# Kernel tuning notes

Hardware: AMD Instinct MI355X
Metric: run time of the kernel (lower is better)

The kernel has to match this reference:

```python
import jax, jax.numpy as jnp
import numpy as np

MARGIN = 1.0
N, D = 4096, 512
NUM_CLASSES = 64


def setup_inputs() -> dict:
    key = jax.random.key(0)
    k1, k2 = jax.random.split(key)
    inputs = jax.random.normal(k1, (N, D), dtype=jnp.float32)
    targets = jax.random.randint(k2, (N,), 0, NUM_CLASSES, dtype=jnp.int64)
    return {"inputs": inputs, "targets": targets}


def reference(inputs, targets):
    n = inputs.shape[0]
    sq = jnp.sum(inputs * inputs, axis=1)  # [n]
    # squared Euclidean distances, clamped at 0 (matches relu in original)
    d2 = jnp.maximum(sq[:, None] + sq[None, :] - 2.0 * (inputs @ inputs.T), 0.0)
    # safe sqrt (zero entries get 0, matching forward; avoids NaN grads)
    dist = jnp.where(d2 > 0, jnp.sqrt(jnp.where(d2 > 0, d2, 1.0)), 0.0)  # [n,n]

    same = targets[:, None] == targets[None, :]
    eye = jnp.eye(n, dtype=bool)
    pos_mask = same & ~eye          # positives, diagonal excluded
    neg_mask = ~same                # negatives (diagonal is same-label, excluded)

    # per-row sum_k exp(margin - d_ik) over negatives  (replaces per-pair loop)
    neg_sum = jnp.sum(jnp.where(neg_mask, jnp.exp(MARGIN - dist), 0.0), axis=1)  # [n]

    # J_ij = log(neg_sum_i + neg_sum_j) + d_ij for positive pairs
    J = jnp.log(neg_sum[:, None] + neg_sum[None, :]) + dist
    triu_pos = jnp.triu(pos_mask)   # loop iterated over upper-triangular positives
    hinge2 = jnp.where(triu_pos, jax.nn.relu(J) ** 2, 0.0)

    # original divides by count of ALL positive entries (both triangles)
    len_p = jnp.sum(pos_mask).astype(jnp.float32)
    return jnp.sum(hinge2) / len_p
```

## Files before the change

kernel.cpp:

```cpp
#include <hip/hip_runtime.h>
#include <math.h>

#define NN 4096
#define DD 512
#define MARGINF 1.0f
#define NCLS 64
#define MAXM 160
#define TRI (MAXM * (MAXM - 1) / 2)
#define NBLK 2080

typedef __attribute__((ext_vector_type(8))) short bf16x8;
typedef __attribute__((ext_vector_type(4))) float f32x4;

#define WS_SQ   0
#define WS_NS   4096
#define WS_LOSS 8192
#define WS_CTR  8193
#define WS_LENP 8194
#define WS_RK   8320
#define WS_MEM  12416
#define WS_XF   32768
#define WS_PD   1081344

__device__ __forceinline__ unsigned short f2bf(float f) {
    unsigned u = __float_as_uint(f);
    u += 0x7fffu + ((u >> 16) & 1u);
    return (unsigned short)(u >> 16);
}

__global__ __launch_bounds__(256) void prep_kernel(const float* __restrict__ X,
                                                   const int* __restrict__ tgt,
                                                   float* __restrict__ ws) {
    __shared__ int tg[NN];
    const int tid = threadIdx.x;
    for (int j = tid; j < NN; j += 256) tg[j] = tgt[j];

    const int wv = tid >> 6, lane = tid & 63;
    const int row = blockIdx.x * 4 + wv;
    const float4* xr = (const float4*)(X + (size_t)row * DD);
    float4 a = xr[2 * lane], b = xr[2 * lane + 1];
    float s = a.x * a.x + a.y * a.y + a.z * a.z + a.w * a.w
            + b.x * b.x + b.y * b.y + b.z * b.z + b.w * b.w;
#pragma unroll
    for (int off = 32; off; off >>= 1) s += __shfl_down(s, off, 64);

    ushort4 pa = {f2bf(a.x), f2bf(a.y), f2bf(a.z), f2bf(a.w)};
    ushort4 pb = {f2bf(b.x), f2bf(b.y), f2bf(b.z), f2bf(b.w)};
    const int r16 = row >> 4, m = row & 15;
    const int kb = lane >> 2, q = lane & 3;
    ushort4* dst = (ushort4*)((unsigned short*)(ws + WS_XF)
                              + ((size_t)(r16 * 16 + kb) * 64 + q * 16 + m) * 8);
    dst[0] = pa;
    dst[1] = pb;

    __syncthreads();
    const int myc = tg[row];
    int cnt = 0;
    for (int j = lane; j < row; j += 64) cnt += (tg[j] == myc) ? 1 : 0;
#pragma unroll
    for (int off = 32; off; off >>= 1) cnt += __shfl_down(cnt, off, 64);
    if (lane == 0) {
        ws[WS_SQ + row] = s;
        ws[WS_NS + row] = 0.0f;
        ((int*)(ws + WS_RK))[row] = cnt;
        if (cnt < MAXM) ((int*)(ws + WS_MEM))[myc * MAXM + cnt] = row;
    }
    if (blockIdx.x == 0 && tid == 0) {
        ws[WS_LOSS] = 0.0f;
        ((unsigned*)ws)[WS_CTR] = 0u;
        ws[WS_LENP] = 0.0f;
    }
}

__global__ __launch_bounds__(256, 5) void negsum_kernel(const int* __restrict__ tgt,
                                                        float* __restrict__ ws) {
    const int bidx = blockIdx.x;
    int bj = (int)((sqrtf(8.0f * (float)bidx + 1.0f) - 1.0f) * 0.5f);
    while (bj * (bj + 1) / 2 > bidx) --bj;
    while ((bj + 1) * (bj + 2) / 2 <= bidx) ++bj;
    const int bi = bidx - bj * (bj + 1) / 2;
    const int i0 = bi * 64, j0 = bj * 64;

    const int tid = threadIdx.x;
    const int w = tid >> 6, lane = tid & 63;
    const int m_ = lane & 15, q = lane >> 4;
    const int wr = (w & 1) * 32, wc = (w >> 1) * 32;
    const unsigned short* Xf = (const unsigned short*)(ws + WS_XF);

    const int air = (i0 + wr) >> 4;
    const int bjr = (j0 + wc) >> 4;
    const unsigned short* pA = Xf + (size_t)air * 8192 + lane * 8;
    const unsigned short* pB = Xf + (size_t)bjr * 8192 + lane * 8;

    f32x4 acc[2][2] = {};
    bf16x8 rgA[3][2], rgB[3][2];
#pragma unroll
    for (int s = 0; s < 2; ++s)
#pragma unroll
        for (int u = 0; u < 2; ++u) {
            rgA[s][u] = *(const bf16x8*)(pA + u * 8192 + s * 512);
            rgB[s][u] = *(const bf16x8*)(pB + u * 8192 + s * 512);
        }
#pragma unroll
    for (int it = 0; it < 16; ++it) {
        const int cur = it % 3, nx = (it + 2) % 3;
        if (it < 14) {
#pragma unroll
            for (int u = 0; u < 2; ++u) {
                rgA[nx][u] = *(const bf16x8*)(pA + u * 8192 + (it + 2) * 512);
                rgB[nx][u] = *(const bf16x8*)(pB + u * 8192 + (it + 2) * 512);
            }
        }
        acc[0][0] = __builtin_amdgcn_mfma_f32_16x16x32_bf16(rgA[cur][0], rgB[cur][0], acc[0][0], 0, 0, 0);
        acc[0][1] = __builtin_amdgcn_mfma_f32_16x16x32_bf16(rgA[cur][0], rgB[cur][1], acc[0][1], 0, 0, 0);
        acc[1][0] = __builtin_amdgcn_mfma_f32_16x16x32_bf16(rgA[cur][1], rgB[cur][0], acc[1][0], 0, 0, 0);
        acc[1][1] = __builtin_amdgcn_mfma_f32_16x16x32_bf16(rgA[cur][1], rgB[cur][1], acc[1][1], 0, 0, 0);
    }

    const float* sq = ws + WS_SQ;
    float* ns = ws + WS_NS;
    const int* rk = (const int*)(ws + WS_RK);
    float* posd = ws + WS_PD;
    float sjv[2]; int tjv[2], jv[2];
#pragma unroll
    for (int v = 0; v < 2; ++v) {
        int j = j0 + wc + v * 16 + m_;
        jv[v] = j;
        sjv[v] = sq[j];
        tjv[v] = tgt[j];
    }
    float colp[2] = {0.0f, 0.0f};
#pragma unroll
    for (int u = 0; u < 2; ++u) {
#pragma unroll
        for (int r = 0; r < 4; ++r) {
            const int i = i0 + wr + u * 16 + q * 4 + r;
            const float si = sq[i];
            const int ti = tgt[i];
            float rp = 0.0f;
#pragma unroll
            for (int v = 0; v < 2; ++v) {
                float d2 = si + sjv[v] - 2.0f * acc[u][v][r];
                float dist = d2 > 0.0f ? sqrtf(d2) : 0.0f;
                if (tjv[v] != ti) {
                    float e = __expf(MARGINF - dist);
                    rp += e;
                    colp[v] += e;
                } else if (i < jv[v]) {
                    int ra = rk[i], rb = rk[jv[v]];
                    if (ra < MAXM && rb < MAXM) {
                        int hi = ra > rb ? ra : rb;
                        int lo = ra > rb ? rb : ra;
                        posd[ti * TRI + hi * (hi - 1) / 2 + lo] = dist;
                    }
                }
            }
            rp += __shfl_xor(rp, 1, 64);
            rp += __shfl_xor(rp, 2, 64);
            rp += __shfl_xor(rp, 4, 64);
            rp += __shfl_xor(rp, 8, 64);
            if (m_ == 0) atomicAdd(&ns[i], rp);
        }
    }
    if (bi != bj) {
#pragma unroll
        for (int v = 0; v < 2; ++v) {
            float cp = colp[v];
            cp += __shfl_xor(cp, 16, 64);
            cp += __shfl_xor(cp, 32, 64);
            if (q == 0) atomicAdd(&ns[jv[v]], cp);
        }
    }
}

__global__ __launch_bounds__(256) void pair2_kernel(const int* __restrict__ tgt,
                                                    float* __restrict__ ws,
                                                    float* __restrict__ out) {
    __shared__ float wsum[4];
    __shared__ int csum[4];
    __shared__ bool last;
    const int c = blockIdx.x;
    const int tid = threadIdx.x;
    const int wv = tid >> 6, lane = tid & 63;

    int ccount = 0;
    for (int j = tid; j < NN; j += 256) ccount += (tgt[j] == c) ? 1 : 0;
#pragma unroll
    for (int off = 32; off; off >>= 1) ccount += __shfl_down(ccount, off, 64);
    if (lane == 0) csum[wv] = ccount;
    __syncthreads();
    int mc = csum[0] + csum[1] + csum[2] + csum[3];
    if (mc > MAXM) mc = MAXM;
    const int P = mc * (mc - 1) / 2;

    const int* mem = (const int*)(ws + WS_MEM) + c * MAXM;
    const float* pd = ws + WS_PD + c * TRI;
    const float* ns = ws + WS_NS;
    float lsum = 0.0f;
    for (int p = tid; p < P; p += 256) {
        int b = (int)((1.0f + sqrtf(1.0f + 8.0f * (float)p)) * 0.5f);
        while (b * (b - 1) / 2 > p) --b;
        while ((b + 1) * b / 2 <= p) ++b;
        const int a = p - b * (b - 1) / 2;
        const float dist = pd[b * (b - 1) / 2 + a];
        const int i = mem[a], j = mem[b];
        float J = __logf(ns[i] + ns[j]) + dist;
        float h = fmaxf(J, 0.0f);
        lsum += h * h;
    }
#pragma unroll
    for (int off = 32; off; off >>= 1) lsum += __shfl_xor(lsum, off, 64);
    if (lane == 0) wsum[wv] = lsum;
    __syncthreads();
    if (tid == 0) {
        float s = wsum[0] + wsum[1] + wsum[2] + wsum[3];
        if (s != 0.0f) atomicAdd(&ws[WS_LOSS], s);
        atomicAdd(&ws[WS_LENP], (float)(mc * (mc - 1)));
        __threadfence();
        unsigned d = atomicAdd((unsigned*)ws + WS_CTR, 1u);
        last = (d == NCLS - 1);
    }
    __syncthreads();
    if (last && tid == 0) {
        float total = atomicAdd(&ws[WS_LOSS], 0.0f);
        float lp = atomicAdd(&ws[WS_LENP], 0.0f);
        out[0] = total / lp;
    }
}

extern "C" void kernel_launch(void* const* d_in, const int* in_sizes, int n_in,
                              void* d_out, int out_size, void* d_ws, size_t ws_size,
                              hipStream_t stream) {
    const float* X  = (const float*)d_in[0];
    const int*  tgt = (const int*)d_in[1];
    float* ws  = (float*)d_ws;
    float* out = (float*)d_out;

    hipLaunchKernelGGL(prep_kernel, dim3(NN / 4), dim3(256), 0, stream, X, tgt, ws);
    hipLaunchKernelGGL(negsum_kernel, dim3(NBLK), dim3(256), 0, stream, tgt, ws);
    hipLaunchKernelGGL(pair2_kernel, dim3(NCLS), dim3(256), 0, stream, tgt, ws, out);
}
```

Measured before the change: 116.0 us.

## Stage 128x128 Gram tiles through LDS and split pair loss across class slices

The distance/negsum kernel moves from 64x64 tiles loaded directly into registers to 128x128 tiles. Operands are staged into double-buffered LDS with global_load_lds, and each wave computes a 4x4 grid of MFMA tiles, which cuts redundant global reads of the bf16 panels. The pair-loss kernel is also split into 4 slices per class, so 256 blocks replace 64 for more parallelism. In exchange, the larger tiles leave fewer blocks (528) and lower occupancy, and the extra block syncs and register pressure could offset the bandwidth savings.

```diff
diff --git a/kernel.cpp b/kernel.cpp
--- a/kernel.cpp
+++ b/kernel.cpp
@@ -7,7 +7,9 @@
 #define NCLS 64
 #define MAXM 160
 #define TRI (MAXM * (MAXM - 1) / 2)
-#define NBLK 2080
+#define PBLK 32
+#define NBLK2 (PBLK * (PBLK + 1) / 2)
+#define NSLICE 4
 
 typedef __attribute__((ext_vector_type(8))) short bf16x8;
 typedef __attribute__((ext_vector_type(4))) float f32x4;
@@ -72,66 +74,85 @@
     }
 }
 
-__global__ __launch_bounds__(256, 5) void negsum_kernel(const int* __restrict__ tgt,
+__device__ __forceinline__ void stage8(const unsigned short* __restrict__ gpanel,
+                                       int t, int fbase, int lane,
+                                       unsigned short* lbase) {
+#pragma unroll
+    for (int s = 0; s < 8; ++s) {
+        const int fi = fbase + s;
+        const unsigned short* gp =
+            gpanel + ((size_t)((fi >> 1) * 16 + t * 2 + (fi & 1))) * 512 + lane * 8;
+        __builtin_amdgcn_global_load_lds(
+            (const __attribute__((address_space(1))) int*)gp,
+            (__attribute__((address_space(3))) int*)(lbase + fi * 512),
+            16, 0, 0);
+    }
+}
+
+__global__ __launch_bounds__(256, 2) void negsum_kernel(const int* __restrict__ tgt,
                                                         float* __restrict__ ws) {
+    __shared__ unsigned short lds[2][2][16][512];
     const int bidx = blockIdx.x;
     int bj = (int)((sqrtf(8.0f * (float)bidx + 1.0f) - 1.0f) * 0.5f);
     while (bj * (bj + 1) / 2 > bidx) --bj;
     while ((bj + 1) * (bj + 2) / 2 <= bidx) ++bj;
     const int bi = bidx - bj * (bj + 1) / 2;
-    const int i0 = bi * 64, j0 = bj * 64;
+    const int i0 = bi * 128, j0 = bj * 128;
 
     const int tid = threadIdx.x;
     const int w = tid >> 6, lane = tid & 63;
     const int m_ = lane & 15, q = lane >> 4;
-    const int wr = (w & 1) * 32, wc = (w >> 1) * 32;
+    const int wr = (w & 1) * 64, wc = (w >> 1) * 64;
     const unsigned short* Xf = (const unsigned short*)(ws + WS_XF);
 
-    const int air = (i0 + wr) >> 4;
-    const int bjr = (j0 + wc) >> 4;
-    const unsigned short* pA = Xf + (size_t)air * 8192 + lane * 8;
-    const unsigned short* pB = Xf + (size_t)bjr * 8192 + lane * 8;
-
-    f32x4 acc[2][2] = {};
-    bf16x8 rgA[3][2], rgB[3][2];
-#pragma unroll
-    for (int s = 0; s < 2; ++s)
-#pragma unroll
-        for (int u = 0; u < 2; ++u) {
-            rgA[s][u] = *(const bf16x8*)(pA + u * 8192 + s * 512);
-            rgB[s][u] = *(const bf16x8*)(pB + u * 8192 + s * 512);
+    const int ab = w >> 1;
+    const int fbase = (w & 1) * 8;
+    const unsigned short* gpanel = Xf + (size_t)(ab ? bj : bi) * 8 * 8192;
+    unsigned short* lb0 = &lds[0][ab][0][0];
+    unsigned short* lb1 = &lds[1][ab][0][0];
+
+    f32x4 acc[4][4] = {};
+
+    stage8(gpanel, 0, fbase, lane, lb0);
+    __syncthreads();
+#pragma unroll 2
+    for (int t = 0; t < 8; ++t) {
+        const int cur = t & 1;
+        if (t < 7) stage8(gpanel, t + 1, fbase, lane, cur ? lb0 : lb1);
+#pragma unroll
+        for (int kbl = 0; kbl < 2; ++kbl) {
+            bf16x8 af[4], bf[4];
+#pragma unroll
+            for (int u = 0; u < 4; ++u)
+                af[u] = *(const bf16x8*)&lds[cur][0][((w & 1) * 4 + u) * 2 + kbl][lane * 8];
+#pragma unroll
+            for (int v = 0; v < 4; ++v)
+                bf[v] = *(const bf16x8*)&lds[cur][1][((w >> 1) * 4 + v) * 2 + kbl][lane * 8];
+#pragma unroll
+            for (int u = 0; u < 4; ++u)
+#pragma unroll
+                for (int v = 0; v < 4; ++v)
+                    acc[u][v] = __builtin_amdgcn_mfma_f32_16x16x32_bf16(
+                        af[u], bf[v], acc[u][v], 0, 0, 0);
         }
-#pragma unroll
-    for (int it = 0; it < 16; ++it) {
-        const int cur = it % 3, nx = (it + 2) % 3;
-        if (it < 14) {
-#pragma unroll
-            for (int u = 0; u < 2; ++u) {
-                rgA[nx][u] = *(const bf16x8*)(pA + u * 8192 + (it + 2) * 512);
-                rgB[nx][u] = *(const bf16x8*)(pB + u * 8192 + (it + 2) * 512);
-            }
-        }
-        acc[0][0] = __builtin_amdgcn_mfma_f32_16x16x32_bf16(rgA[cur][0], rgB[cur][0], acc[0][0], 0, 0, 0);
-        acc[0][1] = __builtin_amdgcn_mfma_f32_16x16x32_bf16(rgA[cur][0], rgB[cur][1], acc[0][1], 0, 0, 0);
-        acc[1][0] = __builtin_amdgcn_mfma_f32_16x16x32_bf16(rgA[cur][1], rgB[cur][0], acc[1][0], 0, 0, 0);
-        acc[1][1] = __builtin_amdgcn_mfma_f32_16x16x32_bf16(rgA[cur][1], rgB[cur][1], acc[1][1], 0, 0, 0);
+        __syncthreads();
     }
 
     const float* sq = ws + WS_SQ;
     float* ns = ws + WS_NS;
     const int* rk = (const int*)(ws + WS_RK);
     float* posd = ws + WS_PD;
-    float sjv[2]; int tjv[2], jv[2];
-#pragma unroll
-    for (int v = 0; v < 2; ++v) {
+    float sjv[4]; int tjv[4], jv[4];
+#pragma unroll
+    for (int v = 0; v < 4; ++v) {
         int j = j0 + wc + v * 16 + m_;
         jv[v] = j;
         sjv[v] = sq[j];
         tjv[v] = tgt[j];
     }
-    float colp[2] = {0.0f, 0.0f};
-#pragma unroll
-    for (int u = 0; u < 2; ++u) {
+    float colp[4] = {0.0f, 0.0f, 0.0f, 0.0f};
+#pragma unroll
+    for (int u = 0; u < 4; ++u) {
 #pragma unroll
         for (int r = 0; r < 4; ++r) {
             const int i = i0 + wr + u * 16 + q * 4 + r;
@@ -139,7 +160,7 @@
             const int ti = tgt[i];
             float rp = 0.0f;
 #pragma unroll
-            for (int v = 0; v < 2; ++v) {
+            for (int v = 0; v < 4; ++v) {
                 float d2 = si + sjv[v] - 2.0f * acc[u][v][r];
                 float dist = d2 > 0.0f ? sqrtf(d2) : 0.0f;
                 if (tjv[v] != ti) {
@@ -164,7 +185,7 @@
     }
     if (bi != bj) {
 #pragma unroll
-        for (int v = 0; v < 2; ++v) {
+        for (int v = 0; v < 4; ++v) {
             float cp = colp[v];
             cp += __shfl_xor(cp, 16, 64);
             cp += __shfl_xor(cp, 32, 64);
@@ -179,7 +200,8 @@
     __shared__ float wsum[4];
     __shared__ int csum[4];
     __shared__ bool last;
-    const int c = blockIdx.x;
+    const int c = blockIdx.x >> 2;
+    const int sl = blockIdx.x & 3;
     const int tid = threadIdx.x;
     const int wv = tid >> 6, lane = tid & 63;
 
@@ -197,7 +219,7 @@
     const float* pd = ws + WS_PD + c * TRI;
     const float* ns = ws + WS_NS;
     float lsum = 0.0f;
-    for (int p = tid; p < P; p += 256) {
+    for (int p = tid + sl * 256; p < P; p += 256 * NSLICE) {
         int b = (int)((1.0f + sqrtf(1.0f + 8.0f * (float)p)) * 0.5f);
         while (b * (b - 1) / 2 > p) --b;
         while ((b + 1) * b / 2 <= p) ++b;
@@ -215,10 +237,10 @@
     if (tid == 0) {
         float s = wsum[0] + wsum[1] + wsum[2] + wsum[3];
         if (s != 0.0f) atomicAdd(&ws[WS_LOSS], s);
-        atomicAdd(&ws[WS_LENP], (float)(mc * (mc - 1)));
+        if (sl == 0) atomicAdd(&ws[WS_LENP], (float)(mc * (mc - 1)));
         __threadfence();
         unsigned d = atomicAdd((unsigned*)ws + WS_CTR, 1u);
-        last = (d == NCLS - 1);
+        last = (d == NCLS * NSLICE - 1);
     }
     __syncthreads();
     if (last && tid == 0) {
@@ -237,6 +259,6 @@
     float* out = (float*)d_out;
 
     hipLaunchKernelGGL(prep_kernel, dim3(NN / 4), dim3(256), 0, stream, X, tgt, ws);
-    hipLaunchKernelGGL(negsum_kernel, dim3(NBLK), dim3(256), 0, stream, tgt, ws);
-    hipLaunchKernelGGL(pair2_kernel, dim3(NCLS), dim3(256), 0, stream, tgt, ws, out);
-}
+    hipLaunchKernelGGL(negsum_kernel, dim3(NBLK2), dim3(256), 0, stream, tgt, ws);
+    hipLaunchKernelGGL(pair2_kernel, dim3(NCLS * NSLICE), dim3(256), 0, stream, tgt, ws, out);
+}
```

Result: slower. 134.7 us (+16.2%).
